# Kernel tuning notes

Measured on AMD Instinct MI355X. Metric: run time of the kernel, lower is better.

Reference implementation:

```python
import jax, jax.numpy as jnp
import numpy as np

E_DIM = 1024
HID = 4096
H = (2 * HID) // 3  # floor(2*hidden/3) = 2730
NUM_EXPERTS = 8
TOP_K = 2
LN_EPS = 1e-5


def setup_inputs() -> dict:
    key = jax.random.key(0)
    ks = jax.random.split(key, 10)
    B, T, P = 2, 8, 256
    s_in = 1.0 / np.sqrt(E_DIM)
    s_h = 1.0 / np.sqrt(H)
    return {
        "x": jax.random.normal(ks[0], (B, T, P, E_DIM), jnp.float32),
        "Wr": jax.random.normal(ks[1], (NUM_EXPERTS, E_DIM), jnp.float32) * s_in,
        "Wv": jax.random.normal(ks[2], (NUM_EXPERTS, E_DIM, H), jnp.float32) * s_in,
        "bv": jax.random.normal(ks[3], (NUM_EXPERTS, H), jnp.float32) * 0.01,
        "Wg": jax.random.normal(ks[4], (NUM_EXPERTS, E_DIM, H), jnp.float32) * s_in,
        "bg": jax.random.normal(ks[5], (NUM_EXPERTS, H), jnp.float32) * 0.01,
        "Wo": jax.random.normal(ks[6], (NUM_EXPERTS, H, E_DIM), jnp.float32) * s_h,
        "bo": jax.random.normal(ks[7], (NUM_EXPERTS, E_DIM), jnp.float32) * 0.01,
        "ln_g": jnp.ones((E_DIM,), jnp.float32),
        "ln_b": jnp.zeros((E_DIM,), jnp.float32),
    }


def reference(x, Wr, Wv, bv, Wg, bg, Wo, bo, ln_g, ln_b):
    B, T, P, E = x.shape
    flat = x.reshape(-1, E)          # [N, E]
    N = flat.shape[0]

    # router: top-k logits -> softmax combine weights
    logits = flat @ Wr.T                              # [N, C]
    tk_vals, tk_idx = jax.lax.top_k(logits, TOP_K)    # [N, K]
    tk_w = jax.nn.softmax(tk_vals, axis=-1)           # [N, K]

    # dense combine-weight matrix: zero for non-routed experts
    comb = jnp.zeros((N, NUM_EXPERTS), flat.dtype)
    comb = comb.at[jnp.arange(N)[:, None], tk_idx].add(tk_w)  # [N, C]

    # all experts over all tokens (masked combine makes this exact)
    hv = jnp.einsum('ne,ceh->cnh', flat, Wv) + bv[:, None, :]  # [C, N, H]
    hg = jnp.einsum('ne,ceh->cnh', flat, Wg) + bg[:, None, :]
    h = jax.nn.silu(hv) * hg                                   # SwiGLU
    oe = jnp.einsum('cnh,che->cne', h, Wo) + bo[:, None, :]    # [C, N, E]
    out = jnp.einsum('cne,nc->ne', oe, comb)                   # weighted combine

    # residual + LayerNorm (AdaptiveNormalizer with no conditioning)
    y = x + out.reshape(B, T, P, E)
    mu = jnp.mean(y, axis=-1, keepdims=True)
    var = jnp.mean((y - mu) ** 2, axis=-1, keepdims=True)
    return ln_g * (y - mu) * jax.lax.rsqrt(var + LN_EPS) + ln_b
```

## Files before the change

kernel.cpp:

```cpp
#include <hip/hip_runtime.h>
#include <hip/hip_bf16.h>

#define E_DIM 1024
#define HDIM  2730
#define HP    2752
#define NEXP  8
#define NTOK  4096
#define NPAIR 8192
#define NSLOT 72
#define LN_EPS 1e-5f

typedef __attribute__((ext_vector_type(8))) short  short8;
typedef __attribute__((ext_vector_type(4))) short  short4v;
typedef __attribute__((ext_vector_type(4))) float  floatx4;
typedef __attribute__((ext_vector_type(4))) int    intx4;

__device__ __forceinline__ __hip_bfloat16 f2bf(float f) { return __float2bfloat16(f); }

__global__ __launch_bounds__(256) void router_k(const float* __restrict__ x,
    const float* __restrict__ Wr, int* __restrict__ counts,
    int* __restrict__ tk_idx, float* __restrict__ tk_w) {
  int wid = threadIdx.x >> 6, lane = threadIdx.x & 63;
  int t = blockIdx.x * 4 + wid;
  const float* xr = x + (size_t)t * E_DIM;
  float xv[16];
#pragma unroll
  for (int i = 0; i < 16; ++i) xv[i] = xr[lane + 64 * i];
  float lg[8];
#pragma unroll
  for (int e = 0; e < 8; ++e) {
    const float* wr = Wr + e * E_DIM;
    float a = 0.f;
#pragma unroll
    for (int i = 0; i < 16; ++i) a += xv[i] * wr[lane + 64 * i];
#pragma unroll
    for (int o = 32; o; o >>= 1) a += __shfl_xor(a, o, 64);
    lg[e] = a;
  }
  if (lane == 0) {
    int i0 = 0; float l0 = lg[0];
#pragma unroll
    for (int e = 1; e < 8; ++e) if (lg[e] > l0) { l0 = lg[e]; i0 = e; }
    int i1 = -1; float l1 = -1e30f;
#pragma unroll
    for (int e = 0; e < 8; ++e) if (e != i0 && lg[e] > l1) { l1 = lg[e]; i1 = e; }
    float w0 = 1.f / (1.f + __expf(l1 - l0));
    atomicAdd(&counts[i0], 1);
    atomicAdd(&counts[i1], 1);
    tk_idx[2 * t]     = i0;  tk_idx[2 * t + 1] = i1;
    tk_w[2 * t]       = w0;  tk_w[2 * t + 1]   = 1.f - w0;
  }
}

__global__ void offsets_k(const int* __restrict__ counts, int* __restrict__ offsets,
                          int* __restrict__ cursor,
                          int* __restrict__ slot_e, int* __restrict__ slot_m0) {
  if (threadIdx.x == 0) {
    int off = 0, s = 0;
    for (int e = 0; e < NEXP; ++e) {
      offsets[e] = off; cursor[e] = off;
      for (int m0 = 0; m0 < counts[e]; m0 += 128) { slot_e[s] = e; slot_m0[s] = m0; ++s; }
      off += counts[e];
    }
    for (; s < NSLOT; ++s) { slot_e[s] = -1; slot_m0[s] = 0; }
  }
}

__global__ __launch_bounds__(256) void scatter_k(const int* __restrict__ tk_idx,
    const float* __restrict__ tk_w, int* __restrict__ cursor,
    int* __restrict__ pair_token, float* __restrict__ pair_w, int* __restrict__ pair_pos) {
  int t = blockIdx.x * 256 + threadIdx.x;
#pragma unroll
  for (int k = 0; k < 2; ++k) {
    int e = tk_idx[2 * t + k];
    int pos = atomicAdd(&cursor[e], 1);
    pair_token[pos] = t;
    pair_w[pos] = tk_w[2 * t + k];
    pair_pos[2 * t + k] = pos;
  }
}

__global__ __launch_bounds__(256) void gatherx_k(const float* __restrict__ x,
    const int* __restrict__ pair_token, __hip_bfloat16* __restrict__ xs) {
  int p = blockIdx.x;
  int t = pair_token[p];
  const float* src = x + (size_t)t * E_DIM;
  __hip_bfloat16* dst = xs + (size_t)p * E_DIM;
  int i = threadIdx.x * 4;
  floatx4 v = *(const floatx4*)(src + i);
  union { __hip_bfloat16 h[4]; short4v s; } u;
#pragma unroll
  for (int j = 0; j < 4; ++j) u.h[j] = f2bf(v[j]);
  *(short4v*)(dst + i) = u.s;
}

__global__ __launch_bounds__(256) void tcvt_k(const float* __restrict__ in,
    __hip_bfloat16* __restrict__ out, int R, int C, int outRS,
    size_t inExpStride, size_t outExpStride) {
  __shared__ float tile[64 * 65];
  int e = blockIdx.z;
  const float* ip = in + inExpStride * e;
  __hip_bfloat16* op = out + outExpStride * e;
  int c0 = blockIdx.x * 64, r0 = blockIdx.y * 64;
#pragma unroll
  for (int i = 0; i < 16; ++i) {
    int idx = i * 256 + threadIdx.x;
    int rr = idx >> 6, cc = idx & 63;
    int gr = r0 + rr, gc = c0 + cc;
    tile[rr * 65 + cc] = (gr < R && gc < C) ? ip[(size_t)gr * C + gc] : 0.f;
  }
  __syncthreads();
#pragma unroll
  for (int i = 0; i < 2; ++i) {
    int idx = i * 256 + threadIdx.x;
    int cc = idx >> 3, rb = (idx & 7) * 8;
    union { __hip_bfloat16 h[8]; intx4 v; } u;
#pragma unroll
    for (int j = 0; j < 8; ++j) u.h[j] = f2bf(tile[(rb + j) * 65 + cc]);
    *(intx4*)(op + (size_t)(c0 + cc) * outRS + (r0 + rb)) = u.v;
  }
}

__global__ __launch_bounds__(256) void gemm1_k(
    const __hip_bfloat16* __restrict__ xs,
    const int* __restrict__ counts, const int* __restrict__ offsets,
    const int* __restrict__ slot_e, const int* __restrict__ slot_m0,
    const float* __restrict__ bv, const float* __restrict__ bg,
    const __hip_bfloat16* __restrict__ WvT, const __hip_bfloat16* __restrict__ WgT,
    __hip_bfloat16* __restrict__ h) {
  int slot = blockIdx.y;
  int e = slot_e[slot];
  if (e < 0) return;
  int m0 = slot_m0[slot];
  int Me = counts[e], off = offsets[e];
  int n0 = blockIdx.x * 64;

  __shared__ __hip_bfloat16 sA[2 * 128 * 40];
  __shared__ __hip_bfloat16 sBv[2 * 64 * 40];
  __shared__ __hip_bfloat16 sBg[2 * 64 * 40];

  int tid = threadIdx.x;
  int wid = tid >> 6, lane = tid & 63;
  int wm = wid >> 1, wn = wid & 1;
  int q = lane >> 4, r = lane & 15;

  int srow = tid >> 3;
  int kk   = (tid & 7) * 8;
  int ks   = kk >> 5, k2 = kk & 31;
  const __hip_bfloat16* gA  = xs + (size_t)(off + m0 + srow) * E_DIM + kk;
  size_t bb = (size_t)e * ((size_t)HP * E_DIM) + (size_t)(n0 + srow) * E_DIM + kk;
  const __hip_bfloat16* gBv = WvT + bb;
  const __hip_bfloat16* gBg = WgT + bb;
  __hip_bfloat16* wA  = sA  + ks * (128 * 40) + srow * 40 + k2;
  __hip_bfloat16* wBv = sBv + ks * (64 * 40) + srow * 40 + k2;
  __hip_bfloat16* wBg = sBg + ks * (64 * 40) + srow * 40 + k2;

  floatx4 accv[4][2], accg[4][2];
  floatx4 zz = {0.f, 0.f, 0.f, 0.f};
#pragma unroll
  for (int mi = 0; mi < 4; ++mi)
#pragma unroll
    for (int ni = 0; ni < 2; ++ni) { accv[mi][ni] = zz; accg[mi][ni] = zz; }

  for (int kt = 0; kt < E_DIM / 64; ++kt) {
    size_t ko = (size_t)kt * 64;
#pragma unroll
    for (int i = 0; i < 4; ++i)
      *(intx4*)(wA + i * 32 * 40) = *(const intx4*)(gA + ko + (size_t)i * 32 * E_DIM);
#pragma unroll
    for (int i = 0; i < 2; ++i) {
      *(intx4*)(wBv + i * 32 * 40) = *(const intx4*)(gBv + ko + (size_t)i * 32 * E_DIM);
      *(intx4*)(wBg + i * 32 * 40) = *(const intx4*)(gBg + ko + (size_t)i * 32 * E_DIM);
    }
    __syncthreads();
#pragma unroll
    for (int s = 0; s < 2; ++s) {
      const __hip_bfloat16* pA  = sA  + s * (128 * 40);
      const __hip_bfloat16* pBv = sBv + s * (64 * 40);
      const __hip_bfloat16* pBg = sBg + s * (64 * 40);
      short8 av[4];
#pragma unroll
      for (int mi = 0; mi < 4; ++mi)
        av[mi] = *(const short8*)(pA + (wm * 64 + mi * 16 + r) * 40 + q * 8);
#pragma unroll
      for (int ni = 0; ni < 2; ++ni) {
        short8 b8v = *(const short8*)(pBv + (wn * 32 + ni * 16 + r) * 40 + q * 8);
        short8 b8g = *(const short8*)(pBg + (wn * 32 + ni * 16 + r) * 40 + q * 8);
#pragma unroll
        for (int mi = 0; mi < 4; ++mi) {
          accv[mi][ni] = __builtin_amdgcn_mfma_f32_16x16x32_bf16(av[mi], b8v, accv[mi][ni], 0, 0, 0);
          accg[mi][ni] = __builtin_amdgcn_mfma_f32_16x16x32_bf16(av[mi], b8g, accg[mi][ni], 0, 0, 0);
        }
      }
    }
    __syncthreads();
  }

#pragma unroll
  for (int mi = 0; mi < 4; ++mi) {
#pragma unroll
    for (int rr = 0; rr < 4; ++rr) {
      int m_loc = wm * 64 + mi * 16 + q * 4 + rr;
      int m = m0 + m_loc;
      if (m >= Me) continue;
      size_t hrow = (size_t)(off + m) * HP;
#pragma unroll
      for (int ni = 0; ni < 2; ++ni) {
        int n = n0 + wn * 32 + ni * 16 + r;
        float bvv = (n < HDIM) ? bv[e * HDIM + n] : 0.f;
        float bgv = (n < HDIM) ? bg[e * HDIM + n] : 0.f;
        float hv = accv[mi][ni][rr] + bvv;
        float hg = accg[mi][ni][rr] + bgv;
        float sgm = 1.f / (1.f + __expf(-hv));
        h[hrow + n] = f2bf(hv * sgm * hg);
      }
    }
  }
}

__global__ __launch_bounds__(256) void gemm2_k(
    const __hip_bfloat16* __restrict__ hb,
    const int* __restrict__ counts, const int* __restrict__ offsets,
    const int* __restrict__ slot_e, const int* __restrict__ slot_m0,
    const float* __restrict__ bo,
    const __hip_bfloat16* __restrict__ WoT,
    float* __restrict__ pout) {
  int slot = blockIdx.y;
  int e = slot_e[slot];
  if (e < 0) return;
  int m0 = slot_m0[slot];
  int Me = counts[e], off = offsets[e];
  int n0 = blockIdx.x * 64;

  __shared__ __hip_bfloat16 sA[2 * 128 * 40];
  __shared__ __hip_bfloat16 sB[2 * 64 * 40];

  int tid = threadIdx.x;
  int wid = tid >> 6, lane = tid & 63;
  int wm = wid >> 1, wn = wid & 1;
  int q = lane >> 4, r = lane & 15;

  int srow = tid >> 3;
  int kk   = (tid & 7) * 8;
  int ks   = kk >> 5, k2 = kk & 31;
  const __hip_bfloat16* gA = hb + (size_t)(off + m0 + srow) * HP + kk;
  const __hip_bfloat16* gB =
      WoT + (size_t)e * ((size_t)E_DIM * HP) + (size_t)(n0 + srow) * HP + kk;
  __hip_bfloat16* wA = sA + ks * (128 * 40) + srow * 40 + k2;
  __hip_bfloat16* wB = sB + ks * (64 * 40) + srow * 40 + k2;

  floatx4 acc[4][2];
  floatx4 zz = {0.f, 0.f, 0.f, 0.f};
#pragma unroll
  for (int mi = 0; mi < 4; ++mi)
#pragma unroll
    for (int ni = 0; ni < 2; ++ni) acc[mi][ni] = zz;

  for (int kt = 0; kt < HP / 64; ++kt) {
    size_t ko = (size_t)kt * 64;
#pragma unroll
    for (int i = 0; i < 4; ++i)
      *(intx4*)(wA + i * 32 * 40) = *(const intx4*)(gA + ko + (size_t)i * 32 * HP);
#pragma unroll
    for (int i = 0; i < 2; ++i)
      *(intx4*)(wB + i * 32 * 40) = *(const intx4*)(gB + ko + (size_t)i * 32 * HP);
    __syncthreads();
#pragma unroll
    for (int s = 0; s < 2; ++s) {
      const __hip_bfloat16* pA = sA + s * (128 * 40);
      const __hip_bfloat16* pB = sB + s * (64 * 40);
      short8 av[4];
#pragma unroll
      for (int mi = 0; mi < 4; ++mi)
        av[mi] = *(const short8*)(pA + (wm * 64 + mi * 16 + r) * 40 + q * 8);
#pragma unroll
      for (int ni = 0; ni < 2; ++ni) {
        short8 b8 = *(const short8*)(pB + (wn * 32 + ni * 16 + r) * 40 + q * 8);
#pragma unroll
        for (int mi = 0; mi < 4; ++mi)
          acc[mi][ni] = __builtin_amdgcn_mfma_f32_16x16x32_bf16(av[mi], b8, acc[mi][ni], 0, 0, 0);
      }
    }
    __syncthreads();
  }

#pragma unroll
  for (int mi = 0; mi < 4; ++mi) {
#pragma unroll
    for (int rr = 0; rr < 4; ++rr) {
      int m_loc = wm * 64 + mi * 16 + q * 4 + rr;
      int m = m0 + m_loc;
      if (m >= Me) continue;
      size_t orow = (size_t)(off + m) * E_DIM;
#pragma unroll
      for (int ni = 0; ni < 2; ++ni) {
        int n = n0 + wn * 32 + ni * 16 + r;
        pout[orow + n] = acc[mi][ni][rr] + bo[e * E_DIM + n];
      }
    }
  }
}

__global__ __launch_bounds__(256) void ln_k(const float* __restrict__ x,
    const float* __restrict__ pout, const int* __restrict__ pair_pos,
    const float* __restrict__ pair_w, const float* __restrict__ ln_g,
    const float* __restrict__ ln_b, float* __restrict__ out) {
  int t = blockIdx.x, tid = threadIdx.x;
  int p0 = pair_pos[2 * t], p1 = pair_pos[2 * t + 1];
  float w0 = pair_w[p0], w1 = pair_w[p1];
  const float* xr = x + (size_t)t * E_DIM;
  const float* r0 = pout + (size_t)p0 * E_DIM;
  const float* r1 = pout + (size_t)p1 * E_DIM;
  float y[4];
  float s = 0.f, ss = 0.f;
#pragma unroll
  for (int i = 0; i < 4; ++i) {
    int e = tid + 256 * i;
    y[i] = xr[e] + w0 * r0[e] + w1 * r1[e];
    s += y[i];
    ss += y[i] * y[i];
  }
#pragma unroll
  for (int o = 32; o; o >>= 1) { s += __shfl_xor(s, o, 64); ss += __shfl_xor(ss, o, 64); }
  __shared__ float red[8];
  int wid = tid >> 6, lane = tid & 63;
  if (lane == 0) { red[wid] = s; red[4 + wid] = ss; }
  __syncthreads();
  s  = red[0] + red[1] + red[2] + red[3];
  ss = red[4] + red[5] + red[6] + red[7];
  float mu = s * (1.f / E_DIM);
  float var = ss * (1.f / E_DIM) - mu * mu;
  float rs = rsqrtf(var + LN_EPS);
#pragma unroll
  for (int i = 0; i < 4; ++i) {
    int e = tid + 256 * i;
    out[(size_t)t * E_DIM + e] = ln_g[e] * (y[i] - mu) * rs + ln_b[e];
  }
}

extern "C" void kernel_launch(void* const* d_in, const int* in_sizes, int n_in,
                              void* d_out, int out_size, void* d_ws, size_t ws_size,
                              hipStream_t stream) {
  const float* x    = (const float*)d_in[0];
  const float* Wr   = (const float*)d_in[1];
  const float* Wv   = (const float*)d_in[2];
  const float* bv   = (const float*)d_in[3];
  const float* Wg   = (const float*)d_in[4];
  const float* bg   = (const float*)d_in[5];
  const float* Wo   = (const float*)d_in[6];
  const float* bo   = (const float*)d_in[7];
  const float* ln_g = (const float*)d_in[8];
  const float* ln_b = (const float*)d_in[9];
  float* out = (float*)d_out;

  char* ws = (char*)d_ws;
  size_t off = 0;
  auto alloc = [&](size_t bytes) -> void* {
    void* p = ws + off;
    off = (off + bytes + 255) & ~(size_t)255;
    return p;
  };
  int*   counts     = (int*)alloc(32);
  int*   cursor     = (int*)alloc(32);
  int*   offsets    = (int*)alloc(32);
  int*   slot_e     = (int*)alloc(NSLOT * 4);
  int*   slot_m0    = (int*)alloc(NSLOT * 4);
  int*   tk_idx     = (int*)alloc((size_t)NTOK * 2 * 4);
  float* tk_w       = (float*)alloc((size_t)NTOK * 2 * 4);
  int*   pair_token = (int*)alloc((size_t)NPAIR * 4);
  float* pair_w     = (float*)alloc((size_t)NPAIR * 4);
  int*   pair_pos   = (int*)alloc((size_t)NPAIR * 4);
  __hip_bfloat16* xs   = (__hip_bfloat16*)alloc((size_t)(NPAIR + 128) * E_DIM * 2);
  __hip_bfloat16* hbuf = (__hip_bfloat16*)alloc((size_t)(NPAIR + 128) * HP * 2);
  float* pout = (float*)alloc((size_t)NPAIR * E_DIM * 4);

  size_t welems = (size_t)NEXP * HP * E_DIM;
  __hip_bfloat16* WvT = (__hip_bfloat16*)alloc(welems * 2);
  __hip_bfloat16* WgT = (__hip_bfloat16*)alloc(welems * 2);
  __hip_bfloat16* WoT = (__hip_bfloat16*)alloc(welems * 2);

  hipMemsetAsync(d_ws, 0, 1024, stream);

  router_k<<<NTOK / 4, 256, 0, stream>>>(x, Wr, counts, tk_idx, tk_w);
  offsets_k<<<1, 64, 0, stream>>>(counts, offsets, cursor, slot_e, slot_m0);
  scatter_k<<<NTOK / 256, 256, 0, stream>>>(tk_idx, tk_w, cursor, pair_token, pair_w, pair_pos);
  gatherx_k<<<NPAIR, 256, 0, stream>>>(x, pair_token, xs);

  tcvt_k<<<dim3(HP / 64, E_DIM / 64, NEXP), 256, 0, stream>>>(
      Wv, WvT, E_DIM, HDIM, E_DIM, (size_t)E_DIM * HDIM, (size_t)HP * E_DIM);
  tcvt_k<<<dim3(HP / 64, E_DIM / 64, NEXP), 256, 0, stream>>>(
      Wg, WgT, E_DIM, HDIM, E_DIM, (size_t)E_DIM * HDIM, (size_t)HP * E_DIM);
  tcvt_k<<<dim3(E_DIM / 64, HP / 64, NEXP), 256, 0, stream>>>(
      Wo, WoT, HDIM, E_DIM, HP, (size_t)HDIM * E_DIM, (size_t)E_DIM * HP);

  gemm1_k<<<dim3(HP / 64, NSLOT), 256, 0, stream>>>(
      xs, counts, offsets, slot_e, slot_m0, bv, bg, WvT, WgT, hbuf);
  gemm2_k<<<dim3(E_DIM / 64, NSLOT), 256, 0, stream>>>(
      hbuf, counts, offsets, slot_e, slot_m0, bo, WoT, pout);

  ln_k<<<NTOK, 256, 0, stream>>>(x, pout, pair_pos, pair_w, ln_g, ln_b, out);
}
```

Measured before the change: 734.3 us.

## Load GEMM tiles directly to LDS with XOR-swizzled unpadded layout

Both expert GEMM kernels now fill shared memory with global_load_lds direct-to-LDS 16-byte loads instead of staging through registers. The padded 40-element row layout is replaced by a dense 64-wide layout with an XOR swizzle of 8-element chunks, applied on both the write and read sides, to avoid bank conflicts. The goal is to cut VGPR pressure and instruction overhead on the load path. The risk is correctness of the swizzle mapping and dependence on compiler support for the builtin and its wait handling before the barrier.

```diff
diff --git a/kernel.cpp b/kernel.cpp
--- a/kernel.cpp
+++ b/kernel.cpp
@@ -16,6 +16,12 @@
 typedef __attribute__((ext_vector_type(4))) int    intx4;
 
 __device__ __forceinline__ __hip_bfloat16 f2bf(float f) { return __float2bfloat16(f); }
+
+__device__ __forceinline__ void gload16(const __hip_bfloat16* g, __hip_bfloat16* l) {
+  __builtin_amdgcn_global_load_lds(
+      (const __attribute__((address_space(1))) void*)(g),
+      (__attribute__((address_space(3))) void*)(l), 16, 0, 0);
+}
 
 __global__ __launch_bounds__(256) void router_k(const float* __restrict__ x,
     const float* __restrict__ Wr, int* __restrict__ counts,
@@ -135,25 +141,52 @@
   int Me = counts[e], off = offsets[e];
   int n0 = blockIdx.x * 64;
 
-  __shared__ __hip_bfloat16 sA[2 * 128 * 40];
-  __shared__ __hip_bfloat16 sBv[2 * 64 * 40];
-  __shared__ __hip_bfloat16 sBg[2 * 64 * 40];
+  __shared__ __align__(16) __hip_bfloat16 sA[128 * 64];
+  __shared__ __align__(16) __hip_bfloat16 sBv[64 * 64];
+  __shared__ __align__(16) __hip_bfloat16 sBg[64 * 64];
 
   int tid = threadIdx.x;
   int wid = tid >> 6, lane = tid & 63;
   int wm = wid >> 1, wn = wid & 1;
   int q = lane >> 4, r = lane & 15;
-
-  int srow = tid >> 3;
-  int kk   = (tid & 7) * 8;
-  int ks   = kk >> 5, k2 = kk & 31;
-  const __hip_bfloat16* gA  = xs + (size_t)(off + m0 + srow) * E_DIM + kk;
-  size_t bb = (size_t)e * ((size_t)HP * E_DIM) + (size_t)(n0 + srow) * E_DIM + kk;
-  const __hip_bfloat16* gBv = WvT + bb;
-  const __hip_bfloat16* gBg = WgT + bb;
-  __hip_bfloat16* wA  = sA  + ks * (128 * 40) + srow * 40 + k2;
-  __hip_bfloat16* wBv = sBv + ks * (64 * 40) + srow * 40 + k2;
-  __hip_bfloat16* wBg = sBg + ks * (64 * 40) + srow * 40 + k2;
+  int key = r & 7;
+
+  int aoff[4][2], boff[2][2];
+#pragma unroll
+  for (int mi = 0; mi < 4; ++mi)
+#pragma unroll
+    for (int s = 0; s < 2; ++s)
+      aoff[mi][s] = (wm * 64 + mi * 16 + r) * 64 + ((((s << 2) + q) ^ key) << 3);
+#pragma unroll
+  for (int ni = 0; ni < 2; ++ni)
+#pragma unroll
+    for (int s = 0; s < 2; ++s)
+      boff[ni][s] = (wn * 32 + ni * 16 + r) * 64 + ((((s << 2) + q) ^ key) << 3);
+
+  int srow8  = lane >> 3;
+  int schunk = (lane & 7) ^ srow8;
+  const __hip_bfloat16* gA[4];
+  __hip_bfloat16* lA[4];
+#pragma unroll
+  for (int i = 0; i < 4; ++i) {
+    int c = i * 4 + wid;
+    gA[i] = xs + (size_t)(off + m0 + c * 8 + srow8) * E_DIM + schunk * 8;
+    lA[i] = sA + c * 512;
+  }
+  const __hip_bfloat16* gBvp[2];
+  const __hip_bfloat16* gBgp[2];
+  __hip_bfloat16* lBv[2];
+  __hip_bfloat16* lBg[2];
+  size_t wb = (size_t)e * ((size_t)HP * E_DIM);
+#pragma unroll
+  for (int i = 0; i < 2; ++i) {
+    int c = i * 4 + wid;
+    size_t rowoff = wb + (size_t)(n0 + c * 8 + srow8) * E_DIM + schunk * 8;
+    gBvp[i] = WvT + rowoff;
+    gBgp[i] = WgT + rowoff;
+    lBv[i] = sBv + c * 512;
+    lBg[i] = sBg + c * 512;
+  }
 
   floatx4 accv[4][2], accg[4][2];
   floatx4 zz = {0.f, 0.f, 0.f, 0.f};
@@ -163,29 +196,25 @@
     for (int ni = 0; ni < 2; ++ni) { accv[mi][ni] = zz; accg[mi][ni] = zz; }
 
   for (int kt = 0; kt < E_DIM / 64; ++kt) {
-    size_t ko = (size_t)kt * 64;
-#pragma unroll
-    for (int i = 0; i < 4; ++i)
-      *(intx4*)(wA + i * 32 * 40) = *(const intx4*)(gA + ko + (size_t)i * 32 * E_DIM);
+    int ko = kt * 64;
+#pragma unroll
+    for (int i = 0; i < 4; ++i) gload16(gA[i] + ko, lA[i]);
 #pragma unroll
     for (int i = 0; i < 2; ++i) {
-      *(intx4*)(wBv + i * 32 * 40) = *(const intx4*)(gBv + ko + (size_t)i * 32 * E_DIM);
-      *(intx4*)(wBg + i * 32 * 40) = *(const intx4*)(gBg + ko + (size_t)i * 32 * E_DIM);
+      gload16(gBvp[i] + ko, lBv[i]);
+      gload16(gBgp[i] + ko, lBg[i]);
     }
     __syncthreads();
 #pragma unroll
     for (int s = 0; s < 2; ++s) {
-      const __hip_bfloat16* pA  = sA  + s * (128 * 40);
-      const __hip_bfloat16* pBv = sBv + s * (64 * 40);
-      const __hip_bfloat16* pBg = sBg + s * (64 * 40);
       short8 av[4];
 #pragma unroll
       for (int mi = 0; mi < 4; ++mi)
-        av[mi] = *(const short8*)(pA + (wm * 64 + mi * 16 + r) * 40 + q * 8);
+        av[mi] = *(const short8*)(sA + aoff[mi][s]);
 #pragma unroll
       for (int ni = 0; ni < 2; ++ni) {
-        short8 b8v = *(const short8*)(pBv + (wn * 32 + ni * 16 + r) * 40 + q * 8);
-        short8 b8g = *(const short8*)(pBg + (wn * 32 + ni * 16 + r) * 40 + q * 8);
+        short8 b8v = *(const short8*)(sBv + boff[ni][s]);
+        short8 b8g = *(const short8*)(sBg + boff[ni][s]);
 #pragma unroll
         for (int mi = 0; mi < 4; ++mi) {
           accv[mi][ni] = __builtin_amdgcn_mfma_f32_16x16x32_bf16(av[mi], b8v, accv[mi][ni], 0, 0, 0);
@@ -232,22 +261,46 @@
   int Me = counts[e], off = offsets[e];
   int n0 = blockIdx.x * 64;
 
-  __shared__ __hip_bfloat16 sA[2 * 128 * 40];
-  __shared__ __hip_bfloat16 sB[2 * 64 * 40];
+  __shared__ __align__(16) __hip_bfloat16 sA[128 * 64];
+  __shared__ __align__(16) __hip_bfloat16 sB[64 * 64];
 
   int tid = threadIdx.x;
   int wid = tid >> 6, lane = tid & 63;
   int wm = wid >> 1, wn = wid & 1;
   int q = lane >> 4, r = lane & 15;
-
-  int srow = tid >> 3;
-  int kk   = (tid & 7) * 8;
-  int ks   = kk >> 5, k2 = kk & 31;
-  const __hip_bfloat16* gA = hb + (size_t)(off + m0 + srow) * HP + kk;
-  const __hip_bfloat16* gB =
-      WoT + (size_t)e * ((size_t)E_DIM * HP) + (size_t)(n0 + srow) * HP + kk;
-  __hip_bfloat16* wA = sA + ks * (128 * 40) + srow * 40 + k2;
-  __hip_bfloat16* wB = sB + ks * (64 * 40) + srow * 40 + k2;
+  int key = r & 7;
+
+  int aoff[4][2], boff[2][2];
+#pragma unroll
+  for (int mi = 0; mi < 4; ++mi)
+#pragma unroll
+    for (int s = 0; s < 2; ++s)
+      aoff[mi][s] = (wm * 64 + mi * 16 + r) * 64 + ((((s << 2) + q) ^ key) << 3);
+#pragma unroll
+  for (int ni = 0; ni < 2; ++ni)
+#pragma unroll
+    for (int s = 0; s < 2; ++s)
+      boff[ni][s] = (wn * 32 + ni * 16 + r) * 64 + ((((s << 2) + q) ^ key) << 3);
+
+  int srow8  = lane >> 3;
+  int schunk = (lane & 7) ^ srow8;
+  const __hip_bfloat16* gA[4];
+  __hip_bfloat16* lA[4];
+#pragma unroll
+  for (int i = 0; i < 4; ++i) {
+    int c = i * 4 + wid;
+    gA[i] = hb + (size_t)(off + m0 + c * 8 + srow8) * HP + schunk * 8;
+    lA[i] = sA + c * 512;
+  }
+  const __hip_bfloat16* gB[2];
+  __hip_bfloat16* lB[2];
+#pragma unroll
+  for (int i = 0; i < 2; ++i) {
+    int c = i * 4 + wid;
+    gB[i] = WoT + (size_t)e * ((size_t)E_DIM * HP) +
+            (size_t)(n0 + c * 8 + srow8) * HP + schunk * 8;
+    lB[i] = sB + c * 512;
+  }
 
   floatx4 acc[4][2];
   floatx4 zz = {0.f, 0.f, 0.f, 0.f};
@@ -257,25 +310,21 @@
     for (int ni = 0; ni < 2; ++ni) acc[mi][ni] = zz;
 
   for (int kt = 0; kt < HP / 64; ++kt) {
-    size_t ko = (size_t)kt * 64;
-#pragma unroll
-    for (int i = 0; i < 4; ++i)
-      *(intx4*)(wA + i * 32 * 40) = *(const intx4*)(gA + ko + (size_t)i * 32 * HP);
-#pragma unroll
-    for (int i = 0; i < 2; ++i)
-      *(intx4*)(wB + i * 32 * 40) = *(const intx4*)(gB + ko + (size_t)i * 32 * HP);
+    int ko = kt * 64;
+#pragma unroll
+    for (int i = 0; i < 4; ++i) gload16(gA[i] + ko, lA[i]);
+#pragma unroll
+    for (int i = 0; i < 2; ++i) gload16(gB[i] + ko, lB[i]);
     __syncthreads();
 #pragma unroll
     for (int s = 0; s < 2; ++s) {
-      const __hip_bfloat16* pA = sA + s * (128 * 40);
-      const __hip_bfloat16* pB = sB + s * (64 * 40);
       short8 av[4];
 #pragma unroll
       for (int mi = 0; mi < 4; ++mi)
-        av[mi] = *(const short8*)(pA + (wm * 64 + mi * 16 + r) * 40 + q * 8);
+        av[mi] = *(const short8*)(sA + aoff[mi][s]);
 #pragma unroll
       for (int ni = 0; ni < 2; ++ni) {
-        short8 b8 = *(const short8*)(pB + (wn * 32 + ni * 16 + r) * 40 + q * 8);
+        short8 b8 = *(const short8*)(sB + boff[ni][s]);
 #pragma unroll
         for (int mi = 0; mi < 4; ++mi)
           acc[mi][ni] = __builtin_amdgcn_mfma_f32_16x16x32_bf16(av[mi], b8, acc[mi][ni], 0, 0, 0);
```

Measured after the change: 726.4 us. About the same (-1.1%).

## Widen GEMM tiles to 128x128 with direct global-to-LDS loads and XOR swizzle

Applied to the files above, without the earlier changes.

Both expert GEMMs move from 128x64 to 128x128 output tiles, with HP padded to a multiple of 128. Tiles are now filled with global_load_lds direct-to-LDS transfers into an unpadded, XOR-swizzled shared layout in place of register-staged padded copies. The aim is more MFMA work per LDS byte, fewer VGPR staging moves and fewer bank conflicts. The cost is higher accumulator register pressure (launch bounds now request 2 blocks per SM), fewer blocks in flight, and larger padded weight buffers that take more conversion work.

```diff
diff --git a/kernel.cpp b/kernel.cpp
--- a/kernel.cpp
+++ b/kernel.cpp
@@ -3,7 +3,7 @@
 
 #define E_DIM 1024
 #define HDIM  2730
-#define HP    2752
+#define HP    2816
 #define NEXP  8
 #define NTOK  4096
 #define NPAIR 8192
@@ -16,6 +16,12 @@
 typedef __attribute__((ext_vector_type(4))) int    intx4;
 
 __device__ __forceinline__ __hip_bfloat16 f2bf(float f) { return __float2bfloat16(f); }
+
+__device__ __forceinline__ void gload16(const __hip_bfloat16* g, __hip_bfloat16* l) {
+  __builtin_amdgcn_global_load_lds(
+      (const __attribute__((address_space(1))) void*)(g),
+      (__attribute__((address_space(3))) void*)(l), 16, 0, 0);
+}
 
 __global__ __launch_bounds__(256) void router_k(const float* __restrict__ x,
     const float* __restrict__ Wr, int* __restrict__ counts,
@@ -121,7 +127,7 @@
   }
 }
 
-__global__ __launch_bounds__(256) void gemm1_k(
+__global__ __launch_bounds__(256, 2) void gemm1_k(
     const __hip_bfloat16* __restrict__ xs,
     const int* __restrict__ counts, const int* __restrict__ offsets,
     const int* __restrict__ slot_e, const int* __restrict__ slot_m0,
@@ -133,59 +139,61 @@
   if (e < 0) return;
   int m0 = slot_m0[slot];
   int Me = counts[e], off = offsets[e];
-  int n0 = blockIdx.x * 64;
-
-  __shared__ __hip_bfloat16 sA[2 * 128 * 40];
-  __shared__ __hip_bfloat16 sBv[2 * 64 * 40];
-  __shared__ __hip_bfloat16 sBg[2 * 64 * 40];
+  int n0 = blockIdx.x * 128;
+
+  __shared__ __align__(16) __hip_bfloat16 sA[128 * 64];
+  __shared__ __align__(16) __hip_bfloat16 sBv[128 * 64];
+  __shared__ __align__(16) __hip_bfloat16 sBg[128 * 64];
 
   int tid = threadIdx.x;
   int wid = tid >> 6, lane = tid & 63;
   int wm = wid >> 1, wn = wid & 1;
   int q = lane >> 4, r = lane & 15;
-
-  int srow = tid >> 3;
-  int kk   = (tid & 7) * 8;
-  int ks   = kk >> 5, k2 = kk & 31;
-  const __hip_bfloat16* gA  = xs + (size_t)(off + m0 + srow) * E_DIM + kk;
-  size_t bb = (size_t)e * ((size_t)HP * E_DIM) + (size_t)(n0 + srow) * E_DIM + kk;
-  const __hip_bfloat16* gBv = WvT + bb;
-  const __hip_bfloat16* gBg = WgT + bb;
-  __hip_bfloat16* wA  = sA  + ks * (128 * 40) + srow * 40 + k2;
-  __hip_bfloat16* wBv = sBv + ks * (64 * 40) + srow * 40 + k2;
-  __hip_bfloat16* wBg = sBg + ks * (64 * 40) + srow * 40 + k2;
-
-  floatx4 accv[4][2], accg[4][2];
+  int key = r & 7;
+
+  int sw[2];
+  sw[0] = ((q ^ key) << 3);
+  sw[1] = (((4 + q) ^ key) << 3);
+  int arow = (wm * 64 + r) * 64;
+  int brow = (wn * 64 + r) * 64;
+
+  int srow8  = lane >> 3;
+  int schunk = (lane & 7) ^ srow8;
+  const __hip_bfloat16* gA0 = xs + (size_t)(off + m0 + wid * 8 + srow8) * E_DIM + schunk * 8;
+  size_t wb = (size_t)e * ((size_t)HP * E_DIM);
+  size_t browoff = wb + (size_t)(n0 + wid * 8 + srow8) * E_DIM + schunk * 8;
+  const __hip_bfloat16* gBv0 = WvT + browoff;
+  const __hip_bfloat16* gBg0 = WgT + browoff;
+  __hip_bfloat16* lA0  = sA  + wid * 512;
+  __hip_bfloat16* lBv0 = sBv + wid * 512;
+  __hip_bfloat16* lBg0 = sBg + wid * 512;
+
+  floatx4 accv[4][4], accg[4][4];
   floatx4 zz = {0.f, 0.f, 0.f, 0.f};
 #pragma unroll
   for (int mi = 0; mi < 4; ++mi)
 #pragma unroll
-    for (int ni = 0; ni < 2; ++ni) { accv[mi][ni] = zz; accg[mi][ni] = zz; }
+    for (int ni = 0; ni < 4; ++ni) { accv[mi][ni] = zz; accg[mi][ni] = zz; }
 
   for (int kt = 0; kt < E_DIM / 64; ++kt) {
-    size_t ko = (size_t)kt * 64;
-#pragma unroll
-    for (int i = 0; i < 4; ++i)
-      *(intx4*)(wA + i * 32 * 40) = *(const intx4*)(gA + ko + (size_t)i * 32 * E_DIM);
-#pragma unroll
-    for (int i = 0; i < 2; ++i) {
-      *(intx4*)(wBv + i * 32 * 40) = *(const intx4*)(gBv + ko + (size_t)i * 32 * E_DIM);
-      *(intx4*)(wBg + i * 32 * 40) = *(const intx4*)(gBg + ko + (size_t)i * 32 * E_DIM);
-    }
+    int ko = kt * 64;
+#pragma unroll
+    for (int i = 0; i < 4; ++i) gload16(gA0  + ko + (size_t)i * 32 * E_DIM, lA0  + i * 2048);
+#pragma unroll
+    for (int i = 0; i < 4; ++i) gload16(gBv0 + ko + (size_t)i * 32 * E_DIM, lBv0 + i * 2048);
+#pragma unroll
+    for (int i = 0; i < 4; ++i) gload16(gBg0 + ko + (size_t)i * 32 * E_DIM, lBg0 + i * 2048);
     __syncthreads();
 #pragma unroll
     for (int s = 0; s < 2; ++s) {
-      const __hip_bfloat16* pA  = sA  + s * (128 * 40);
-      const __hip_bfloat16* pBv = sBv + s * (64 * 40);
-      const __hip_bfloat16* pBg = sBg + s * (64 * 40);
       short8 av[4];
 #pragma unroll
       for (int mi = 0; mi < 4; ++mi)
-        av[mi] = *(const short8*)(pA + (wm * 64 + mi * 16 + r) * 40 + q * 8);
-#pragma unroll
-      for (int ni = 0; ni < 2; ++ni) {
-        short8 b8v = *(const short8*)(pBv + (wn * 32 + ni * 16 + r) * 40 + q * 8);
-        short8 b8g = *(const short8*)(pBg + (wn * 32 + ni * 16 + r) * 40 + q * 8);
+        av[mi] = *(const short8*)(sA + arow + mi * 16 * 64 + sw[s]);
+#pragma unroll
+      for (int ni = 0; ni < 4; ++ni) {
+        short8 b8v = *(const short8*)(sBv + brow + ni * 16 * 64 + sw[s]);
+        short8 b8g = *(const short8*)(sBg + brow + ni * 16 * 64 + sw[s]);
 #pragma unroll
         for (int mi = 0; mi < 4; ++mi) {
           accv[mi][ni] = __builtin_amdgcn_mfma_f32_16x16x32_bf16(av[mi], b8v, accv[mi][ni], 0, 0, 0);
@@ -196,6 +204,13 @@
     __syncthreads();
   }
 
+  float bvv[4], bgv[4];
+#pragma unroll
+  for (int ni = 0; ni < 4; ++ni) {
+    int n = n0 + wn * 64 + ni * 16 + r;
+    bvv[ni] = (n < HDIM) ? bv[e * HDIM + n] : 0.f;
+    bgv[ni] = (n < HDIM) ? bg[e * HDIM + n] : 0.f;
+  }
 #pragma unroll
   for (int mi = 0; mi < 4; ++mi) {
 #pragma unroll
@@ -205,12 +220,10 @@
       if (m >= Me) continue;
       size_t hrow = (size_t)(off + m) * HP;
 #pragma unroll
-      for (int ni = 0; ni < 2; ++ni) {
-        int n = n0 + wn * 32 + ni * 16 + r;
-        float bvv = (n < HDIM) ? bv[e * HDIM + n] : 0.f;
-        float bgv = (n < HDIM) ? bg[e * HDIM + n] : 0.f;
-        float hv = accv[mi][ni][rr] + bvv;
-        float hg = accg[mi][ni][rr] + bgv;
+      for (int ni = 0; ni < 4; ++ni) {
+        int n = n0 + wn * 64 + ni * 16 + r;
+        float hv = accv[mi][ni][rr] + bvv[ni];
+        float hg = accg[mi][ni][rr] + bgv[ni];
         float sgm = 1.f / (1.f + __expf(-hv));
         h[hrow + n] = f2bf(hv * sgm * hg);
       }
@@ -230,52 +243,54 @@
   if (e < 0) return;
   int m0 = slot_m0[slot];
   int Me = counts[e], off = offsets[e];
-  int n0 = blockIdx.x * 64;
-
-  __shared__ __hip_bfloat16 sA[2 * 128 * 40];
-  __shared__ __hip_bfloat16 sB[2 * 64 * 40];
+  int n0 = blockIdx.x * 128;
+
+  __shared__ __align__(16) __hip_bfloat16 sA[128 * 64];
+  __shared__ __align__(16) __hip_bfloat16 sB[128 * 64];
 
   int tid = threadIdx.x;
   int wid = tid >> 6, lane = tid & 63;
   int wm = wid >> 1, wn = wid & 1;
   int q = lane >> 4, r = lane & 15;
-
-  int srow = tid >> 3;
-  int kk   = (tid & 7) * 8;
-  int ks   = kk >> 5, k2 = kk & 31;
-  const __hip_bfloat16* gA = hb + (size_t)(off + m0 + srow) * HP + kk;
-  const __hip_bfloat16* gB =
-      WoT + (size_t)e * ((size_t)E_DIM * HP) + (size_t)(n0 + srow) * HP + kk;
-  __hip_bfloat16* wA = sA + ks * (128 * 40) + srow * 40 + k2;
-  __hip_bfloat16* wB = sB + ks * (64 * 40) + srow * 40 + k2;
-
-  floatx4 acc[4][2];
+  int key = r & 7;
+
+  int sw[2];
+  sw[0] = ((q ^ key) << 3);
+  sw[1] = (((4 + q) ^ key) << 3);
+  int arow = (wm * 64 + r) * 64;
+  int brow = (wn * 64 + r) * 64;
+
+  int srow8  = lane >> 3;
+  int schunk = (lane & 7) ^ srow8;
+  const __hip_bfloat16* gA0 = hb + (size_t)(off + m0 + wid * 8 + srow8) * HP + schunk * 8;
+  const __hip_bfloat16* gB0 = WoT + (size_t)e * ((size_t)E_DIM * HP) +
+                              (size_t)(n0 + wid * 8 + srow8) * HP + schunk * 8;
+  __hip_bfloat16* lA0 = sA + wid * 512;
+  __hip_bfloat16* lB0 = sB + wid * 512;
+
+  floatx4 acc[4][4];
   floatx4 zz = {0.f, 0.f, 0.f, 0.f};
 #pragma unroll
   for (int mi = 0; mi < 4; ++mi)
 #pragma unroll
-    for (int ni = 0; ni < 2; ++ni) acc[mi][ni] = zz;
+    for (int ni = 0; ni < 4; ++ni) acc[mi][ni] = zz;
 
   for (int kt = 0; kt < HP / 64; ++kt) {
-    size_t ko = (size_t)kt * 64;
-#pragma unroll
-    for (int i = 0; i < 4; ++i)
-      *(intx4*)(wA + i * 32 * 40) = *(const intx4*)(gA + ko + (size_t)i * 32 * HP);
-#pragma unroll
-    for (int i = 0; i < 2; ++i)
-      *(intx4*)(wB + i * 32 * 40) = *(const intx4*)(gB + ko + (size_t)i * 32 * HP);
+    int ko = kt * 64;
+#pragma unroll
+    for (int i = 0; i < 4; ++i) gload16(gA0 + ko + (size_t)i * 32 * HP, lA0 + i * 2048);
+#pragma unroll
+    for (int i = 0; i < 4; ++i) gload16(gB0 + ko + (size_t)i * 32 * HP, lB0 + i * 2048);
     __syncthreads();
 #pragma unroll
     for (int s = 0; s < 2; ++s) {
-      const __hip_bfloat16* pA = sA + s * (128 * 40);
-      const __hip_bfloat16* pB = sB + s * (64 * 40);
       short8 av[4];
 #pragma unroll
       for (int mi = 0; mi < 4; ++mi)
-        av[mi] = *(const short8*)(pA + (wm * 64 + mi * 16 + r) * 40 + q * 8);
-#pragma unroll
-      for (int ni = 0; ni < 2; ++ni) {
-        short8 b8 = *(const short8*)(pB + (wn * 32 + ni * 16 + r) * 40 + q * 8);
+        av[mi] = *(const short8*)(sA + arow + mi * 16 * 64 + sw[s]);
+#pragma unroll
+      for (int ni = 0; ni < 4; ++ni) {
+        short8 b8 = *(const short8*)(sB + brow + ni * 16 * 64 + sw[s]);
 #pragma unroll
         for (int mi = 0; mi < 4; ++mi)
           acc[mi][ni] = __builtin_amdgcn_mfma_f32_16x16x32_bf16(av[mi], b8, acc[mi][ni], 0, 0, 0);
@@ -293,8 +308,8 @@
       if (m >= Me) continue;
       size_t orow = (size_t)(off + m) * E_DIM;
 #pragma unroll
-      for (int ni = 0; ni < 2; ++ni) {
-        int n = n0 + wn * 32 + ni * 16 + r;
+      for (int ni = 0; ni < 4; ++ni) {
+        int n = n0 + wn * 64 + ni * 16 + r;
         pout[orow + n] = acc[mi][ni][rr] + bo[e * E_DIM + n];
       }
     }
@@ -393,9 +408,9 @@
   tcvt_k<<<dim3(E_DIM / 64, HP / 64, NEXP), 256, 0, stream>>>(
       Wo, WoT, HDIM, E_DIM, HP, (size_t)HDIM * E_DIM, (size_t)E_DIM * HP);
 
-  gemm1_k<<<dim3(HP / 64, NSLOT), 256, 0, stream>>>(
+  gemm1_k<<<dim3(HP / 128, NSLOT), 256, 0, stream>>>(
       xs, counts, offsets, slot_e, slot_m0, bv, bg, WvT, WgT, hbuf);
-  gemm2_k<<<dim3(E_DIM / 64, NSLOT), 256, 0, stream>>>(
+  gemm2_k<<<dim3(E_DIM / 128, NSLOT), 256, 0, stream>>>(
       hbuf, counts, offsets, slot_e, slot_m0, bo, WoT, pout);
 
   ln_k<<<NTOK, 256, 0, stream>>>(x, pout, pair_pos, pair_w, ln_g, ln_b, out);
```

Result: faster. 674.1 us (-8.2%).
